# Kernel tuning notes

Measured on AMD Instinct MI355X. Metric: run time of the kernel, lower is better.

Reference implementation:

```python
import jax, jax.numpy as jnp
import numpy as np

B, T, IN_DIM, LATENT, NUM_TOKENS = 8, 2048, 1024, 256, 4096


def setup_inputs() -> dict:
    key = jax.random.key(0)
    k1, k2, k3 = jax.random.split(key, 3)
    x = jax.random.normal(k1, (B, T, IN_DIM), dtype=jnp.float32)
    # Linear projection params (Kaiming-ish scale)
    W = jax.random.normal(k2, (IN_DIM, LATENT), dtype=jnp.float32) / np.sqrt(IN_DIM)
    b = jnp.zeros((LATENT,), dtype=jnp.float32)
    # Codebook (nn.Embedding with xavier_uniform init ~ small normal here)
    codebook = jax.random.normal(k3, (NUM_TOKENS, LATENT), dtype=jnp.float32) * 0.05
    return {"x": x, "W": W, "b": b, "codebook": codebook}


def reference(x, W, b, codebook):
    # normalization='none' -> identity; projection: Linear(in_dim, latent_dim)
    h = jnp.einsum("btd,de->bte", x, W) + b              # [B,T,latent]
    flat = h.reshape(-1, h.shape[-1])                     # [N,latent]
    # cdist + argmin: squared distance gives identical argmin as euclidean
    # d2[n,k] = |flat[n]|^2 - 2 flat@cb^T + |cb[k]|^2
    d2 = (jnp.sum(flat * flat, axis=-1, keepdims=True)
          - 2.0 * (flat @ codebook.T)
          + jnp.sum(codebook * codebook, axis=-1))        # [N,num_tokens]
    indices = jnp.argmin(d2, axis=-1)                     # [N]
    codes = codebook[indices].reshape(h.shape)            # gather -> [B,T,latent]
    idx = indices.reshape(x.shape[:-1] + (1,))            # [B,T,1]
    return codes, idx
```

## Files before the change

kernel.cpp:

```cpp
#include <hip/hip_runtime.h>

#define NROWS   16384
#define INDIM   1024
#define KDIM    256
#define NCODES  4096
#define G_ROWS  32
#define V_ROWS  64
#define P_ROWS  128
#define NSTEP   128

#define VBUF    32768

#define MG_ROWS 64
#define MG_KC   64
#define MG_NCH  (INDIM / MG_KC)
#define XP(p)   ((p) * 8192)
#define WP(p)   (24576 + (p) * 32768)
#define MG_LDS  122880

typedef float f32x4 __attribute__((ext_vector_type(4)));
typedef int   i32x2 __attribute__((ext_vector_type(2)));
typedef short short8 __attribute__((ext_vector_type(8)));
typedef unsigned short u16x8 __attribute__((ext_vector_type(8)));
typedef unsigned short u16x4 __attribute__((ext_vector_type(4)));

__device__ inline unsigned short f2bf(float f) {
    unsigned u = __builtin_bit_cast(unsigned, f);
    u = (u + 0x7fffu + ((u >> 16) & 1u)) >> 16;
    return (unsigned short)u;
}
__device__ inline float bf2f(unsigned short h) {
    unsigned u = ((unsigned)h) << 16;
    return __builtin_bit_cast(float, u);
}
__device__ inline f32x4 mfma16(u16x8 a, u16x8 b, f32x4 c) {
    return __builtin_amdgcn_mfma_f32_16x16x32_bf16(
        __builtin_bit_cast(short8, a), __builtin_bit_cast(short8, b), c, 0, 0, 0);
}

__global__ __launch_bounds__(256) void wprep_kernel(const float* __restrict__ W,
                                                    unsigned short* __restrict__ wt_hi,
                                                    unsigned short* __restrict__ wt_md,
                                                    unsigned short* __restrict__ wt_lo) {
    const int t = threadIdx.x;
    const int k = blockIdx.x * 4 + (t >> 6);
    const int c0 = (t & 63) * 4;
    f32x4 v = *(const f32x4*)(W + (size_t)k * KDIM + c0);
    #pragma unroll
    for (int i = 0; i < 4; ++i) {
        const unsigned short h = f2bf(v[i]);
        const float r1 = v[i] - bf2f(h);
        const unsigned short m = f2bf(r1);
        const unsigned short lo = f2bf(r1 - bf2f(m));
        wt_hi[(size_t)(c0 + i) * INDIM + k] = h;
        wt_md[(size_t)(c0 + i) * INDIM + k] = m;
        wt_lo[(size_t)(c0 + i) * INDIM + k] = lo;
    }
}

__global__ __launch_bounds__(256, 1) void gemm_mfma_kernel(const float* __restrict__ x,
                                                           const unsigned short* __restrict__ wt_hi,
                                                           const unsigned short* __restrict__ wt_md,
                                                           const unsigned short* __restrict__ wt_lo,
                                                           const float* __restrict__ bvec,
                                                           float* __restrict__ hbuf) {
    __shared__ __align__(16) char lds[MG_LDS];

    const int t  = threadIdx.x;
    const int w  = t >> 6;
    const int l  = t & 63;
    const int nl = l & 15;
    const int g  = l >> 4;
    const size_t n0 = (size_t)blockIdx.x * MG_ROWS;
    const int lb = l * 16;

    f32x4 acc[4][4];
    #pragma unroll
    for (int a = 0; a < 4; ++a)
        #pragma unroll
        for (int b = 0; b < 4; ++b) acc[a][b] = (f32x4){0.f, 0.f, 0.f, 0.f};

    for (int kc = 0; kc < MG_NCH; ++kc) {
        f32x4 xa[2], xb[2];
        #pragma unroll
        for (int c = 0; c < 2; ++c) {
            const int idx = w * 2 + c;
            const int sX = idx >> 2, rsX = idx & 3;
            const float* p = x + (n0 + rsX * 16 + nl) * INDIM + kc * MG_KC + sX * 32 + g * 8;
            xa[c] = *(const f32x4*)(p);
            xb[c] = *(const f32x4*)(p + 4);
        }
        u16x8 wh[8], wm[8], wl[8];
        #pragma unroll
        for (int ci = 0; ci < 4; ++ci)
            #pragma unroll
            for (int sW = 0; sW < 2; ++sW) {
                const int q = ci * 2 + sW;
                const size_t off = (size_t)((w * 4 + ci) * 16 + nl) * INDIM
                                 + kc * MG_KC + sW * 32 + g * 8;
                wh[q] = *(const u16x8*)(wt_hi + off);
                wm[q] = *(const u16x8*)(wt_md + off);
                wl[q] = *(const u16x8*)(wt_lo + off);
            }
        __syncthreads();

        #pragma unroll
        for (int c = 0; c < 2; ++c) {
            const int idx = w * 2 + c;
            const int sX = idx >> 2, rsX = idx & 3;
            u16x8 xh, xm, xl;
            #pragma unroll
            for (int e = 0; e < 4; ++e) {
                const float a0 = xa[c][e], a1 = xb[c][e];
                const unsigned short h0 = f2bf(a0);
                const float r10 = a0 - bf2f(h0);
                const unsigned short m0 = f2bf(r10);
                const unsigned short l0 = f2bf(r10 - bf2f(m0));
                const unsigned short h1 = f2bf(a1);
                const float r11 = a1 - bf2f(h1);
                const unsigned short m1 = f2bf(r11);
                const unsigned short l1 = f2bf(r11 - bf2f(m1));
                xh[e] = h0; xh[4+e] = h1;
                xm[e] = m0; xm[4+e] = m1;
                xl[e] = l0; xl[4+e] = l1;
            }
            const int base = (sX * 4 + rsX) * 1024 + lb;
            *(u16x8*)(lds + XP(0) + base) = xh;
            *(u16x8*)(lds + XP(1) + base) = xm;
            *(u16x8*)(lds + XP(2) + base) = xl;
        }
        #pragma unroll
        for (int ci = 0; ci < 4; ++ci)
            #pragma unroll
            for (int sW = 0; sW < 2; ++sW) {
                const int q = ci * 2 + sW;
                const int base = (sW * 16 + w * 4 + ci) * 1024 + lb;
                *(u16x8*)(lds + WP(0) + base) = wh[q];
                *(u16x8*)(lds + WP(1) + base) = wm[q];
                *(u16x8*)(lds + WP(2) + base) = wl[q];
            }
        __syncthreads();

        #pragma unroll
        for (int s = 0; s < 2; ++s) {
            u16x8 bh[4], bm[4], bl[4], ah[4], am[4], al[4];
            #pragma unroll
            for (int rs = 0; rs < 4; ++rs) {
                const int base = (s * 4 + rs) * 1024 + lb;
                bh[rs] = *(const u16x8*)(lds + XP(0) + base);
                bm[rs] = *(const u16x8*)(lds + XP(1) + base);
                bl[rs] = *(const u16x8*)(lds + XP(2) + base);
            }
            #pragma unroll
            for (int ct = 0; ct < 4; ++ct) {
                const int base = (s * 16 + w * 4 + ct) * 1024 + lb;
                ah[ct] = *(const u16x8*)(lds + WP(0) + base);
                am[ct] = *(const u16x8*)(lds + WP(1) + base);
                al[ct] = *(const u16x8*)(lds + WP(2) + base);
            }
            #pragma unroll
            for (int ct = 0; ct < 4; ++ct)
                #pragma unroll
                for (int rs = 0; rs < 4; ++rs) {
                    acc[ct][rs] = mfma16(ah[ct], bh[rs], acc[ct][rs]);
                    acc[ct][rs] = mfma16(ah[ct], bm[rs], acc[ct][rs]);
                    acc[ct][rs] = mfma16(am[ct], bh[rs], acc[ct][rs]);
                    acc[ct][rs] = mfma16(ah[ct], bl[rs], acc[ct][rs]);
                    acc[ct][rs] = mfma16(al[ct], bh[rs], acc[ct][rs]);
                    acc[ct][rs] = mfma16(am[ct], bm[rs], acc[ct][rs]);
                }
        }
    }

    #pragma unroll
    for (int ct = 0; ct < 4; ++ct) {
        float bv[4];
        #pragma unroll
        for (int r = 0; r < 4; ++r) bv[r] = bvec[w * 64 + ct * 16 + g * 4 + r];
        #pragma unroll
        for (int rs = 0; rs < 4; ++rs) {
            const size_t row = n0 + rs * 16 + nl;
            #pragma unroll
            for (int r = 0; r < 4; ++r)
                hbuf[row * KDIM + w * 64 + ct * 16 + g * 4 + r] = acc[ct][rs][r] + bv[r];
        }
    }
}

__global__ __launch_bounds__(256, 2) void gemm_fb_kernel(const float* __restrict__ x,
                                                         const float* __restrict__ W,
                                                         const float* __restrict__ bvec,
                                                         float* __restrict__ hbuf) {
    const int t  = threadIdx.x;
    const int cg = t & 15;
    const int rg = t >> 4;
    const size_t n0 = (size_t)blockIdx.x * G_ROWS;
    const int c0 = cg * 16;

    float acc[2][16];
    #pragma unroll
    for (int j = 0; j < 2; ++j)
        #pragma unroll
        for (int cc = 0; cc < 16; ++cc) acc[j][cc] = 0.f;

    for (int k4 = 0; k4 < INDIM / 4; ++k4) {
        const int k = k4 * 4;
        f32x4 xv[2];
        #pragma unroll
        for (int j = 0; j < 2; ++j)
            xv[j] = *(const f32x4*)(x + (n0 + rg + 16 * j) * INDIM + k);
        f32x4 wv[4][4];
        #pragma unroll
        for (int kk = 0; kk < 4; ++kk)
            #pragma unroll
            for (int q = 0; q < 4; ++q)
                wv[kk][q] = *(const f32x4*)(W + (size_t)(k + kk) * KDIM + c0 + 4 * q);
        #pragma unroll
        for (int j = 0; j < 2; ++j)
            #pragma unroll
            for (int kk = 0; kk < 4; ++kk) {
                const float xs = xv[j][kk];
                #pragma unroll
                for (int q = 0; q < 4; ++q)
                    #pragma unroll
                    for (int e = 0; e < 4; ++e)
                        acc[j][4*q+e] = fmaf(xs, wv[kk][q][e], acc[j][4*q+e]);
            }
    }
    #pragma unroll
    for (int j = 0; j < 2; ++j) {
        float* dst = hbuf + (n0 + rg + 16 * j) * KDIM + c0;
        #pragma unroll
        for (int q = 0; q < 4; ++q) {
            f32x4 v;
            #pragma unroll
            for (int e = 0; e < 4; ++e) v[e] = acc[j][4*q+e] + bvec[c0 + 4*q + e];
            *(f32x4*)(dst + 4*q) = v;
        }
    }
}

__global__ __launch_bounds__(256) void prep_kernel(const float* __restrict__ cb,
                                                   float* __restrict__ cnorm,
                                                   unsigned short* __restrict__ cb_hi,
                                                   unsigned short* __restrict__ cb_lo,
                                                   int do_split) {
    const int c    = blockIdx.x * 4 + (threadIdx.x >> 6);
    const int lane = threadIdx.x & 63;
    f32x4 v = ((const f32x4*)(cb + (size_t)c * KDIM))[lane];
    if (do_split) {
        u16x4 h4, l4;
        #pragma unroll
        for (int j = 0; j < 4; ++j) {
            unsigned short h = f2bf(v[j]);
            h4[j] = h;
            l4[j] = f2bf(v[j] - bf2f(h));
        }
        *(u16x4*)(cb_hi + (size_t)c * KDIM + lane * 4) = h4;
        *(u16x4*)(cb_lo + (size_t)c * KDIM + lane * 4) = l4;
    }
    float s = v[0]*v[0] + v[1]*v[1] + v[2]*v[2] + v[3]*v[3];
    #pragma unroll
    for (int off = 1; off < 64; off <<= 1) s += __shfl_xor(s, off);
    if (lane == 0) cnorm[c] = s;
}

template<int PRE>
__global__ __launch_bounds__(256, 2) void vq_partial_kernel(
    const float* __restrict__ hbuf,
    const float* __restrict__ cb,
    const float* __restrict__ cnorm,
    const unsigned short* __restrict__ cb_hi,
    const unsigned short* __restrict__ cb_lo,
    int* __restrict__ recs)
{
    __shared__ __align__(16) char lds[2 * VBUF];

    const int t  = threadIdx.x;
    const int w  = t >> 6;
    const int l  = t & 63;
    const int nl = l & 15;
    const int g  = l >> 4;
    const int lb = l * 16;
    const int bid  = blockIdx.x;
    const int quar = bid & 3;
    const int S0   = quar * 32;
    const size_t n0 = (size_t)(bid >> 2) * P_ROWS;

    u16x8 bhi[2][8], bmid[2][8];
    #pragma unroll
    for (int rset = 0; rset < 2; ++rset) {
        const float* hrow = hbuf + (n0 + w * 32 + rset * 16 + nl) * KDIM;
        #pragma unroll
        for (int s = 0; s < 8; ++s) {
            f32x4 a = *(const f32x4*)(hrow + s * 32 + g * 8);
            f32x4 b = *(const f32x4*)(hrow + s * 32 + g * 8 + 4);
            u16x8 uh, um;
            #pragma unroll
            for (int jj = 0; jj < 4; ++jj) {
                unsigned short h0 = f2bf(a[jj]); uh[jj]   = h0; um[jj]   = f2bf(a[jj] - bf2f(h0));
                unsigned short h1 = f2bf(b[jj]); uh[4+jj] = h1; um[4+jj] = f2bf(b[jj] - bf2f(h1));
            }
            bhi[rset][s] = uh; bmid[rset][s] = um;
        }
    }

    float v1[2] = {3.4e38f, 3.4e38f}, v2[2] = {3.4e38f, 3.4e38f};
    int   i1[2] = {0, 0},            i2[2] = {0, 0};

    u16x8 rh[2][2], rl[2][2];

    #pragma unroll
    for (int t2 = 0; t2 < 2; ++t2)
        #pragma unroll
        for (int sv = 0; sv < 2; ++sv) {
            const int sst = w * 2 + sv;
            const int code = S0 * 32 + t2 * 16 + nl;
            if (PRE) {
                const size_t off = (size_t)code * KDIM + (sst * 4 + g) * 8;
                rh[t2][sv] = *(const u16x8*)(cb_hi + off);
                rl[t2][sv] = *(const u16x8*)(cb_lo + off);
            } else {
                const float* p = cb + (size_t)code * KDIM + (sst * 4 + g) * 8;
                f32x4 a = *(const f32x4*)(p);
                f32x4 b = *(const f32x4*)(p + 4);
                u16x8 uh, ul;
                #pragma unroll
                for (int jj = 0; jj < 4; ++jj) {
                    unsigned short h0 = f2bf(a[jj]); uh[jj]   = h0; ul[jj]   = f2bf(a[jj] - bf2f(h0));
                    unsigned short h1 = f2bf(b[jj]); uh[4+jj] = h1; ul[4+jj] = f2bf(b[jj] - bf2f(h1));
                }
                rh[t2][sv] = uh; rl[t2][sv] = ul;
            }
        }
    #pragma unroll
    for (int t2 = 0; t2 < 2; ++t2)
        #pragma unroll
        for (int sv = 0; sv < 2; ++sv) {
            const int base = (t2 * 8 + w * 2 + sv) * 1024 + lb;
            *(u16x8*)(lds + base) = rh[t2][sv];
            *(u16x8*)(lds + 16384 + base) = rl[t2][sv];
        }
    __syncthreads();

    for (int S = S0; S < S0 + 32; ++S) {
        const int b = S & 1;
        if (S + 1 < S0 + 32) {
            #pragma unroll
            for (int t2 = 0; t2 < 2; ++t2)
                #pragma unroll
                for (int sv = 0; sv < 2; ++sv) {
                    const int sst = w * 2 + sv;
                    const int code = (S + 1) * 32 + t2 * 16 + nl;
                    if (PRE) {
                        const size_t off = (size_t)code * KDIM + (sst * 4 + g) * 8;
                        rh[t2][sv] = *(const u16x8*)(cb_hi + off);
                        rl[t2][sv] = *(const u16x8*)(cb_lo + off);
                    } else {
                        const float* p = cb + (size_t)code * KDIM + (sst * 4 + g) * 8;
                        f32x4 a = *(const f32x4*)(p);
                        f32x4 bb = *(const f32x4*)(p + 4);
                        u16x8 uh, ul;
                        #pragma unroll
                        for (int jj = 0; jj < 4; ++jj) {
                            unsigned short h0 = f2bf(a[jj]);  uh[jj]   = h0; ul[jj]   = f2bf(a[jj] - bf2f(h0));
                            unsigned short h1 = f2bf(bb[jj]); uh[4+jj] = h1; ul[4+jj] = f2bf(bb[jj] - bf2f(h1));
                        }
                        rh[t2][sv] = uh; rl[t2][sv] = ul;
                    }
                }
        }
        f32x4 cn0 = *(const f32x4*)(cnorm + S * 32 + g * 4);
        f32x4 cn1 = *(const f32x4*)(cnorm + S * 32 + 16 + g * 4);
        {
            const char* buf = lds + b * VBUF;
            #pragma unroll
            for (int t2 = 0; t2 < 2; ++t2) {
                f32x4 acc0 = {0.f, 0.f, 0.f, 0.f};
                f32x4 acc1 = {0.f, 0.f, 0.f, 0.f};
                #pragma unroll
                for (int s = 0; s < 8; ++s) {
                    const int base = (t2 * 8 + s) * 1024 + lb;
                    u16x8 ahi = *(const u16x8*)(buf + base);
                    u16x8 alo = *(const u16x8*)(buf + 16384 + base);
                    acc0 = mfma16(ahi, bhi[0][s],  acc0);
                    acc0 = mfma16(ahi, bmid[0][s], acc0);
                    acc0 = mfma16(alo, bhi[0][s],  acc0);
                    acc1 = mfma16(ahi, bhi[1][s],  acc1);
                    acc1 = mfma16(ahi, bmid[1][s], acc1);
                    acc1 = mfma16(alo, bhi[1][s],  acc1);
                }
                const f32x4 cn = t2 ? cn1 : cn0;
                #pragma unroll
                for (int r = 0; r < 4; ++r) {
                    const int c = S * 32 + t2 * 16 + g * 4 + r;
                    const float d0 = cn[r] - 2.0f * acc0[r];
                    if (d0 < v1[0])      { v2[0] = v1[0]; i2[0] = i1[0]; v1[0] = d0; i1[0] = c; }
                    else if (d0 < v2[0]) { v2[0] = d0; i2[0] = c; }
                    const float d1 = cn[r] - 2.0f * acc1[r];
                    if (d1 < v1[1])      { v2[1] = v1[1]; i2[1] = i1[1]; v1[1] = d1; i1[1] = c; }
                    else if (d1 < v2[1]) { v2[1] = d1; i2[1] = c; }
                }
            }
        }
        __syncthreads();
        if (S + 1 < S0 + 32) {
            char* nbuf = lds + (b ^ 1) * VBUF;
            #pragma unroll
            for (int t2 = 0; t2 < 2; ++t2)
                #pragma unroll
                for (int sv = 0; sv < 2; ++sv) {
                    const int base = (t2 * 8 + w * 2 + sv) * 1024 + lb;
                    *(u16x8*)(nbuf + base) = rh[t2][sv];
                    *(u16x8*)(nbuf + 16384 + base) = rl[t2][sv];
                }
        }
        __syncthreads();
    }

    #pragma unroll
    for (int rset = 0; rset < 2; ++rset) {
        #pragma unroll
        for (int off = 16; off <= 32; off <<= 1) {
            float ov1 = __shfl_xor(v1[rset], off); int oi1 = __shfl_xor(i1[rset], off);
            float ov2 = __shfl_xor(v2[rset], off); int oi2 = __shfl_xor(i2[rset], off);
            if (ov1 < v1[rset] || (ov1 == v1[rset] && oi1 < i1[rset])) {
                float tv = v1[rset]; int ti = i1[rset]; v1[rset] = ov1; i1[rset] = oi1; ov1 = tv; oi1 = ti;
                tv = v2[rset]; ti = i2[rset]; v2[rset] = ov2; i2[rset] = oi2; ov2 = tv; oi2 = ti;
            }
            if (ov1 < v2[rset] || (ov1 == v2[rset] && oi1 < i2[rset])) { v2[rset] = ov1; i2[rset] = oi1; }
        }
    }

    if (g == 0) {
        #pragma unroll
        for (int rset = 0; rset < 2; ++rset) {
            i32x2 rec;
            rec[0] = i1[rset]; rec[1] = i2[rset];
            const size_t row = n0 + w * 32 + rset * 16 + nl;
            *(i32x2*)(recs + (row * 4 + quar) * 2) = rec;
        }
    }
}

__global__ __launch_bounds__(256) void vq_merge_kernel(
    float* __restrict__ hbuf,
    const float* __restrict__ cb,
    const float* __restrict__ cnorm,
    const int* __restrict__ recs,
    float* __restrict__ idx_out)
{
    const int t  = threadIdx.x;
    const int w  = t >> 6;
    const int l  = t & 63;
    const int nl = l & 15;
    const int g  = l >> 4;
    const size_t n0 = (size_t)blockIdx.x * V_ROWS;
    const int row = w * 16 + nl;
    float* hrow = hbuf + (n0 + row) * KDIM;

    int cand[8];
    {
        const size_t rb = (n0 + row) * 8;
        #pragma unroll
        for (int q = 0; q < 4; ++q) {
            i32x2 rq = *(const i32x2*)(recs + rb + q * 2);
            int a = rq[0], b = rq[1];
            cand[2*q]   = (a < 0) ? 0 : (a > NCODES - 1 ? NCODES - 1 : a);
            cand[2*q+1] = (b < 0) ? 0 : (b > NCODES - 1 ? NCODES - 1 : b);
        }
    }

    f32x4 hreg[16];
    #pragma unroll
    for (int s = 0; s < 8; ++s) {
        hreg[2*s]   = *(const f32x4*)(hrow + s * 32 + g * 8);
        hreg[2*s+1] = *(const f32x4*)(hrow + s * 32 + g * 8 + 4);
    }

    float bestd = 3.4e38f;
    int   besti = 0x7fffffff;
    #pragma unroll
    for (int k = 0; k < 8; ++k) {
        const int ci = cand[k];
        const float* cp = cb + (size_t)ci * KDIM;
        float d = 0.f;
        #pragma unroll
        for (int s = 0; s < 8; ++s) {
            f32x4 a = *(const f32x4*)(cp + s * 32 + g * 8);
            f32x4 b = *(const f32x4*)(cp + s * 32 + g * 8 + 4);
            #pragma unroll
            for (int jj = 0; jj < 4; ++jj) {
                d = fmaf(a[jj], hreg[2*s][jj], d);
                d = fmaf(b[jj], hreg[2*s+1][jj], d);
            }
        }
        d += __shfl_xor(d, 16); d += __shfl_xor(d, 32);
        const float d2 = cnorm[ci] - 2.f * d;
        if (d2 < bestd || (d2 == bestd && ci < besti)) { bestd = d2; besti = ci; }
    }

    const float* cw = cb + (size_t)besti * KDIM;
    #pragma unroll
    for (int s = 0; s < 8; ++s) {
        *(f32x4*)(hrow + s * 32 + g * 8)     = *(const f32x4*)(cw + s * 32 + g * 8);
        *(f32x4*)(hrow + s * 32 + g * 8 + 4) = *(const f32x4*)(cw + s * 32 + g * 8 + 4);
    }
    if (g == 0) idx_out[n0 + row] = (float)besti;
}

template<int PRE>
__global__ __launch_bounds__(256) void vq_kernel(
    float* __restrict__ hbuf,
    const float* __restrict__ cb,
    const float* __restrict__ cnorm,
    const unsigned short* __restrict__ cb_hi,
    const unsigned short* __restrict__ cb_lo,
    float* __restrict__ idx_out)
{
    __shared__ __align__(16) char lds[2 * VBUF];

    const int t  = threadIdx.x;
    const int w  = t >> 6;
    const int l  = t & 63;
    const int nl = l & 15;
    const int g  = l >> 4;
    const int lb = l * 16;
    const size_t n0 = (size_t)blockIdx.x * V_ROWS;
    const int row = w * 16 + nl;
    float* hrow = hbuf + (n0 + row) * KDIM;

    u16x8 bhi[8], bmid[8];
    #pragma unroll
    for (int s = 0; s < 8; ++s) {
        f32x4 a = *(const f32x4*)(hrow + s * 32 + g * 8);
        f32x4 b = *(const f32x4*)(hrow + s * 32 + g * 8 + 4);
        u16x8 uh, um;
        #pragma unroll
        for (int jj = 0; jj < 4; ++jj) {
            unsigned short h0 = f2bf(a[jj]); uh[jj]   = h0; um[jj]   = f2bf(a[jj] - bf2f(h0));
            unsigned short h1 = f2bf(b[jj]); uh[4+jj] = h1; um[4+jj] = f2bf(b[jj] - bf2f(h1));
        }
        bhi[s] = uh; bmid[s] = um;
    }

    float v1 = 3.4e38f, v2 = 3.4e38f;
    int   i1 = 0, i2 = 0;

    u16x8 rh[2][2], rl[2][2];

    #pragma unroll
    for (int t2 = 0; t2 < 2; ++t2)
        #pragma unroll
        for (int sv = 0; sv < 2; ++sv) {
            const int sst = w * 2 + sv;
            if (PRE) {
                const size_t off = (size_t)(t2 * 16 + nl) * KDIM + (sst * 4 + g) * 8;
                rh[t2][sv] = *(const u16x8*)(cb_hi + off);
                rl[t2][sv] = *(const u16x8*)(cb_lo + off);
            } else {
                const float* p = cb + (size_t)(t2 * 16 + nl) * KDIM + (sst * 4 + g) * 8;
                f32x4 a = *(const f32x4*)(p);
                f32x4 b = *(const f32x4*)(p + 4);
                u16x8 uh, ul;
                #pragma unroll
                for (int jj = 0; jj < 4; ++jj) {
                    unsigned short h0 = f2bf(a[jj]); uh[jj]   = h0; ul[jj]   = f2bf(a[jj] - bf2f(h0));
                    unsigned short h1 = f2bf(b[jj]); uh[4+jj] = h1; ul[4+jj] = f2bf(b[jj] - bf2f(h1));
                }
                rh[t2][sv] = uh; rl[t2][sv] = ul;
            }
        }
    #pragma unroll
    for (int t2 = 0; t2 < 2; ++t2)
        #pragma unroll
        for (int sv = 0; sv < 2; ++sv) {
            const int base = (t2 * 8 + w * 2 + sv) * 1024 + lb;
            *(u16x8*)(lds + base) = rh[t2][sv];
            *(u16x8*)(lds + 16384 + base) = rl[t2][sv];
        }
    __syncthreads();

    for (int S = 0; S < NSTEP; ++S) {
        const int b = S & 1;
        if (S + 1 < NSTEP) {
            #pragma unroll
            for (int t2 = 0; t2 < 2; ++t2)
                #pragma unroll
                for (int sv = 0; sv < 2; ++sv) {
                    const int sst = w * 2 + sv;
                    const int code = (S + 1) * 32 + t2 * 16 + nl;
                    if (PRE) {
                        const size_t off = (size_t)code * KDIM + (sst * 4 + g) * 8;
                        rh[t2][sv] = *(const u16x8*)(cb_hi + off);
                        rl[t2][sv] = *(const u16x8*)(cb_lo + off);
                    } else {
                        const float* p = cb + (size_t)code * KDIM + (sst * 4 + g) * 8;
                        f32x4 a = *(const f32x4*)(p);
                        f32x4 bb = *(const f32x4*)(p + 4);
                        u16x8 uh, ul;
                        #pragma unroll
                        for (int jj = 0; jj < 4; ++jj) {
                            unsigned short h0 = f2bf(a[jj]);  uh[jj]   = h0; ul[jj]   = f2bf(a[jj] - bf2f(h0));
                            unsigned short h1 = f2bf(bb[jj]); uh[4+jj] = h1; ul[4+jj] = f2bf(bb[jj] - bf2f(h1));
                        }
                        rh[t2][sv] = uh; rl[t2][sv] = ul;
                    }
                }
        }
        f32x4 cn0 = *(const f32x4*)(cnorm + S * 32 + g * 4);
        f32x4 cn1 = *(const f32x4*)(cnorm + S * 32 + 16 + g * 4);
        {
            const char* buf = lds + b * VBUF;
            #pragma unroll
            for (int t2 = 0; t2 < 2; ++t2) {
                f32x4 acc = {0.f, 0.f, 0.f, 0.f};
                #pragma unroll
                for (int s = 0; s < 8; ++s) {
                    const int base = (t2 * 8 + s) * 1024 + lb;
                    u16x8 ahi = *(const u16x8*)(buf + base);
                    u16x8 alo = *(const u16x8*)(buf + 16384 + base);
                    acc = mfma16(ahi, bhi[s],  acc);
                    acc = mfma16(ahi, bmid[s], acc);
                    acc = mfma16(alo, bhi[s],  acc);
                }
                const f32x4 cn = t2 ? cn1 : cn0;
                #pragma unroll
                for (int r = 0; r < 4; ++r) {
                    const float d2 = cn[r] - 2.0f * acc[r];
                    const int c = S * 32 + t2 * 16 + g * 4 + r;
                    if (d2 < v1)      { v2 = v1; i2 = i1; v1 = d2; i1 = c; }
                    else if (d2 < v2) { v2 = d2; i2 = c; }
                }
            }
        }
        __syncthreads();
        if (S + 1 < NSTEP) {
            char* nbuf = lds + (b ^ 1) * VBUF;
            #pragma unroll
            for (int t2 = 0; t2 < 2; ++t2)
                #pragma unroll
                for (int sv = 0; sv < 2; ++sv) {
                    const int base = (t2 * 8 + w * 2 + sv) * 1024 + lb;
                    *(u16x8*)(nbuf + base) = rh[t2][sv];
                    *(u16x8*)(nbuf + 16384 + base) = rl[t2][sv];
                }
        }
        __syncthreads();
    }

    #pragma unroll
    for (int off = 16; off <= 32; off <<= 1) {
        float ov1 = __shfl_xor(v1, off); int oi1 = __shfl_xor(i1, off);
        float ov2 = __shfl_xor(v2, off); int oi2 = __shfl_xor(i2, off);
        if (ov1 < v1 || (ov1 == v1 && oi1 < i1)) {
            float tv = v1; int ti = i1; v1 = ov1; i1 = oi1; ov1 = tv; oi1 = ti;
            tv = v2; ti = i2; v2 = ov2; i2 = oi2; ov2 = tv; oi2 = ti;
        }
        if (ov1 < v2 || (ov1 == v2 && oi1 < i2)) { v2 = ov1; i2 = oi1; }
    }

    i1 = (i1 < 0) ? 0 : (i1 > NCODES - 1 ? NCODES - 1 : i1);
    i2 = (i2 < 0) ? 0 : (i2 > NCODES - 1 ? NCODES - 1 : i2);

    const float* cp1 = cb + (size_t)i1 * KDIM;
    const float* cp2 = cb + (size_t)i2 * KDIM;
    float da = 0.f, db = 0.f;
    #pragma unroll
    for (int s = 0; s < 8; ++s) {
        f32x4 h0 = *(const f32x4*)(hrow + s * 32 + g * 8);
        f32x4 h1 = *(const f32x4*)(hrow + s * 32 + g * 8 + 4);
        f32x4 a1 = *(const f32x4*)(cp1 + s * 32 + g * 8);
        f32x4 b1 = *(const f32x4*)(cp1 + s * 32 + g * 8 + 4);
        f32x4 a2 = *(const f32x4*)(cp2 + s * 32 + g * 8);
        f32x4 b2 = *(const f32x4*)(cp2 + s * 32 + g * 8 + 4);
        #pragma unroll
        for (int jj = 0; jj < 4; ++jj) {
            da = fmaf(a1[jj], h0[jj], da); da = fmaf(b1[jj], h1[jj], da);
            db = fmaf(a2[jj], h0[jj], db); db = fmaf(b2[jj], h1[jj], db);
        }
    }
    da += __shfl_xor(da, 16); da += __shfl_xor(da, 32);
    db += __shfl_xor(db, 16); db += __shfl_xor(db, 32);
    const float d2a = cnorm[i1] - 2.f * da;
    const float d2b = cnorm[i2] - 2.f * db;
    const int win = (d2a < d2b || (d2a == d2b && i1 < i2)) ? i1 : i2;

    const float* cw = cb + (size_t)win * KDIM;
    #pragma unroll
    for (int s = 0; s < 8; ++s) {
        *(f32x4*)(hrow + s * 32 + g * 8)     = *(const f32x4*)(cw + s * 32 + g * 8);
        *(f32x4*)(hrow + s * 32 + g * 8 + 4) = *(const f32x4*)(cw + s * 32 + g * 8 + 4);
    }
    if (g == 0) idx_out[n0 + row] = (float)win;
}

extern "C" void kernel_launch(void* const* d_in, const int* in_sizes, int n_in,
                              void* d_out, int out_size, void* d_ws, size_t ws_size,
                              hipStream_t stream) {
    (void)in_sizes; (void)n_in; (void)out_size;
    const float* x    = (const float*)d_in[0];
    const float* W    = (const float*)d_in[1];
    const float* bvec = (const float*)d_in[2];
    const float* cb   = (const float*)d_in[3];

    float* codes_out = (float*)d_out;
    float* idx_out   = (float*)d_out + (size_t)NROWS * KDIM;

    float* cnorm = (float*)d_ws;
    int*   recs  = (int*)((char*)d_ws + 16384);
    unsigned short* cb_hi = (unsigned short*)((char*)d_ws + 16384 + 524288);
    unsigned short* cb_lo = cb_hi + (size_t)NCODES * KDIM;
    unsigned short* wt_hi = cb_lo + (size_t)NCODES * KDIM;
    unsigned short* wt_md = wt_hi + (size_t)INDIM * KDIM;
    unsigned short* wt_lo = wt_md + (size_t)INDIM * KDIM;

    const size_t need_rec  = 16384 + 524288;
    const size_t need_cb   = need_rec + (size_t)NCODES * KDIM * 2 * sizeof(unsigned short);
    const size_t need_full = need_cb + (size_t)INDIM * KDIM * 3 * sizeof(unsigned short);

    const int use_split = (ws_size >= need_rec) ? 1 : 0;
    const int pre_cb    = (ws_size >= need_cb) ? 1 : 0;
    const int fast_g    = (ws_size >= need_full) ? 1 : 0;

    if (fast_g) {
        wprep_kernel<<<INDIM / 4, 256, 0, stream>>>(W, wt_hi, wt_md, wt_lo);
        gemm_mfma_kernel<<<NROWS / MG_ROWS, 256, 0, stream>>>(x, wt_hi, wt_md, wt_lo, bvec, codes_out);
    } else {
        gemm_fb_kernel<<<NROWS / G_ROWS, 256, 0, stream>>>(x, W, bvec, codes_out);
    }
    prep_kernel<<<NCODES / 4, 256, 0, stream>>>(cb, cnorm, cb_hi, cb_lo, pre_cb);

    if (use_split) {
        if (pre_cb)
            vq_partial_kernel<1><<<(NROWS / P_ROWS) * 4, 256, 0, stream>>>(codes_out, cb, cnorm, cb_hi, cb_lo, recs);
        else
            vq_partial_kernel<0><<<(NROWS / P_ROWS) * 4, 256, 0, stream>>>(codes_out, cb, cnorm, cb_hi, cb_lo, recs);
        vq_merge_kernel<<<NROWS / V_ROWS, 256, 0, stream>>>(codes_out, cb, cnorm, recs, idx_out);
    } else {
        if (pre_cb)
            vq_kernel<1><<<NROWS / V_ROWS, 256, 0, stream>>>(codes_out, cb, cnorm, cb_hi, cb_lo, idx_out);
        else
            vq_kernel<0><<<NROWS / V_ROWS, 256, 0, stream>>>(codes_out, cb, cnorm, cb_hi, cb_lo, idx_out);
    }
}
```

Baseline: 262.3 us.

## Use direct global-to-LDS loads with smaller codebook tiles in VQ partial kernel

The partial VQ search kernel now streams 16 codes per step instead of 32, which halves its LDS footprint. The launch bound rises from 2 to 4 blocks per CU. In the precomputed path, codebook hi/lo tiles are fetched with global_load_lds, so data goes straight to shared memory without passing through registers, and the second barrier per step is dropped. The aim is to raise occupancy and cut register and LDS-store traffic, at the cost of twice as many loop iterations and barriers per block.

```diff
diff --git a/kernel.cpp b/kernel.cpp
--- a/kernel.cpp
+++ b/kernel.cpp
@@ -7,8 +7,10 @@
 #define G_ROWS  32
 #define V_ROWS  64
 #define P_ROWS  128
+#define PSTEP   64
 #define NSTEP   128
 
+#define PVBUF   16384
 #define VBUF    32768
 
 #define MG_ROWS 64
@@ -36,6 +38,13 @@
 __device__ inline f32x4 mfma16(u16x8 a, u16x8 b, f32x4 c) {
     return __builtin_amdgcn_mfma_f32_16x16x32_bf16(
         __builtin_bit_cast(short8, a), __builtin_bit_cast(short8, b), c, 0, 0, 0);
+}
+
+__device__ inline void gload16(const void* g, void* l) {
+    __builtin_amdgcn_global_load_lds(
+        (const __attribute__((address_space(1))) unsigned int*)g,
+        (__attribute__((address_space(3))) unsigned int*)l,
+        16, 0, 0);
 }
 
 __global__ __launch_bounds__(256) void wprep_kernel(const float* __restrict__ W,
@@ -266,7 +275,7 @@
 }
 
 template<int PRE>
-__global__ __launch_bounds__(256, 2) void vq_partial_kernel(
+__global__ __launch_bounds__(256, 4) void vq_partial_kernel(
     const float* __restrict__ hbuf,
     const float* __restrict__ cb,
     const float* __restrict__ cnorm,
@@ -274,7 +283,7 @@
     const unsigned short* __restrict__ cb_lo,
     int* __restrict__ recs)
 {
-    __shared__ __align__(16) char lds[2 * VBUF];
+    __shared__ __align__(16) char lds[2 * PVBUF];
 
     const int t  = threadIdx.x;
     const int w  = t >> 6;
@@ -284,7 +293,7 @@
     const int lb = l * 16;
     const int bid  = blockIdx.x;
     const int quar = bid & 3;
-    const int S0   = quar * 32;
+    const int cbase = quar * 1024;
     const size_t n0 = (size_t)(bid >> 2) * P_ROWS;
 
     u16x8 bhi[2][8], bmid[2][8];
@@ -308,6 +317,240 @@
     float v1[2] = {3.4e38f, 3.4e38f}, v2[2] = {3.4e38f, 3.4e38f};
     int   i1[2] = {0, 0},            i2[2] = {0, 0};
 
+    u16x8 rh[2], rl[2];
+
+    if (PRE) {
+        #pragma unroll
+        for (int sv = 0; sv < 2; ++sv) {
+            const int sc = w * 2 + sv;
+            const size_t off = (size_t)(cbase + nl) * KDIM + (sc * 4 + g) * 8;
+            gload16(cb_hi + off, lds + sc * 1024);
+            gload16(cb_lo + off, lds + 8192 + sc * 1024);
+        }
+    } else {
+        #pragma unroll
+        for (int sv = 0; sv < 2; ++sv) {
+            const int sc = w * 2 + sv;
+            const float* p = cb + (size_t)(cbase + nl) * KDIM + (sc * 4 + g) * 8;
+            f32x4 a = *(const f32x4*)(p);
+            f32x4 b = *(const f32x4*)(p + 4);
+            u16x8 uh, ul;
+            #pragma unroll
+            for (int jj = 0; jj < 4; ++jj) {
+                unsigned short h0 = f2bf(a[jj]); uh[jj]   = h0; ul[jj]   = f2bf(a[jj] - bf2f(h0));
+                unsigned short h1 = f2bf(b[jj]); uh[4+jj] = h1; ul[4+jj] = f2bf(b[jj] - bf2f(h1));
+            }
+            rh[sv] = uh; rl[sv] = ul;
+        }
+        #pragma unroll
+        for (int sv = 0; sv < 2; ++sv) {
+            const int sc = w * 2 + sv;
+            *(u16x8*)(lds + sc * 1024 + lb) = rh[sv];
+            *(u16x8*)(lds + 8192 + sc * 1024 + lb) = rl[sv];
+        }
+    }
+    __syncthreads();
+
+    for (int S = 0; S < PSTEP; ++S) {
+        const int b = S & 1;
+        char* nbuf = lds + (b ^ 1) * PVBUF;
+        if (S + 1 < PSTEP) {
+            if (PRE) {
+                #pragma unroll
+                for (int sv = 0; sv < 2; ++sv) {
+                    const int sc = w * 2 + sv;
+                    const size_t off = (size_t)(cbase + (S + 1) * 16 + nl) * KDIM + (sc * 4 + g) * 8;
+                    gload16(cb_hi + off, nbuf + sc * 1024);
+                    gload16(cb_lo + off, nbuf + 8192 + sc * 1024);
+                }
+            } else {
+                #pragma unroll
+                for (int sv = 0; sv < 2; ++sv) {
+                    const int sc = w * 2 + sv;
+                    const float* p = cb + (size_t)(cbase + (S + 1) * 16 + nl) * KDIM + (sc * 4 + g) * 8;
+                    f32x4 a = *(const f32x4*)(p);
+                    f32x4 bb = *(const f32x4*)(p + 4);
+                    u16x8 uh, ul;
+                    #pragma unroll
+                    for (int jj = 0; jj < 4; ++jj) {
+                        unsigned short h0 = f2bf(a[jj]);  uh[jj]   = h0; ul[jj]   = f2bf(a[jj] - bf2f(h0));
+                        unsigned short h1 = f2bf(bb[jj]); uh[4+jj] = h1; ul[4+jj] = f2bf(bb[jj] - bf2f(h1));
+                    }
+                    rh[sv] = uh; rl[sv] = ul;
+                }
+            }
+        }
+        const f32x4 cn = *(const f32x4*)(cnorm + cbase + S * 16 + g * 4);
+        {
+            const char* buf = lds + b * PVBUF;
+            f32x4 acc0 = {0.f, 0.f, 0.f, 0.f};
+            f32x4 acc1 = {0.f, 0.f, 0.f, 0.f};
+            #pragma unroll
+            for (int s = 0; s < 8; ++s) {
+                const int base = s * 1024 + lb;
+                u16x8 ahi = *(const u16x8*)(buf + base);
+                u16x8 alo = *(const u16x8*)(buf + 8192 + base);
+                acc0 = mfma16(ahi, bhi[0][s],  acc0);
+                acc0 = mfma16(ahi, bmid[0][s], acc0);
+                acc0 = mfma16(alo, bhi[0][s],  acc0);
+                acc1 = mfma16(ahi, bhi[1][s],  acc1);
+                acc1 = mfma16(ahi, bmid[1][s], acc1);
+                acc1 = mfma16(alo, bhi[1][s],  acc1);
+            }
+            #pragma unroll
+            for (int r = 0; r < 4; ++r) {
+                const int c = cbase + S * 16 + g * 4 + r;
+                const float d0 = cn[r] - 2.0f * acc0[r];
+                if (d0 < v1[0])      { v2[0] = v1[0]; i2[0] = i1[0]; v1[0] = d0; i1[0] = c; }
+                else if (d0 < v2[0]) { v2[0] = d0; i2[0] = c; }
+                const float d1 = cn[r] - 2.0f * acc1[r];
+                if (d1 < v1[1])      { v2[1] = v1[1]; i2[1] = i1[1]; v1[1] = d1; i1[1] = c; }
+                else if (d1 < v2[1]) { v2[1] = d1; i2[1] = c; }
+            }
+        }
+        __syncthreads();
+        if (!PRE) {
+            if (S + 1 < PSTEP) {
+                #pragma unroll
+                for (int sv = 0; sv < 2; ++sv) {
+                    const int sc = w * 2 + sv;
+                    *(u16x8*)(nbuf + sc * 1024 + lb) = rh[sv];
+                    *(u16x8*)(nbuf + 8192 + sc * 1024 + lb) = rl[sv];
+                }
+            }
+            __syncthreads();
+        }
+    }
+
+    #pragma unroll
+    for (int rset = 0; rset < 2; ++rset) {
+        #pragma unroll
+        for (int off = 16; off <= 32; off <<= 1) {
+            float ov1 = __shfl_xor(v1[rset], off); int oi1 = __shfl_xor(i1[rset], off);
+            float ov2 = __shfl_xor(v2[rset], off); int oi2 = __shfl_xor(i2[rset], off);
+            if (ov1 < v1[rset] || (ov1 == v1[rset] && oi1 < i1[rset])) {
+                float tv = v1[rset]; int ti = i1[rset]; v1[rset] = ov1; i1[rset] = oi1; ov1 = tv; oi1 = ti;
+                tv = v2[rset]; ti = i2[rset]; v2[rset] = ov2; i2[rset] = oi2; ov2 = tv; oi2 = ti;
+            }
+            if (ov1 < v2[rset] || (ov1 == v2[rset] && oi1 < i2[rset])) { v2[rset] = ov1; i2[rset] = oi1; }
+        }
+    }
+
+    if (g == 0) {
+        #pragma unroll
+        for (int rset = 0; rset < 2; ++rset) {
+            i32x2 rec;
+            rec[0] = i1[rset]; rec[1] = i2[rset];
+            const size_t row = n0 + w * 32 + rset * 16 + nl;
+            *(i32x2*)(recs + (row * 4 + quar) * 2) = rec;
+        }
+    }
+}
+
+__global__ __launch_bounds__(256) void vq_merge_kernel(
+    float* __restrict__ hbuf,
+    const float* __restrict__ cb,
+    const float* __restrict__ cnorm,
+    const int* __restrict__ recs,
+    float* __restrict__ idx_out)
+{
+    const int t  = threadIdx.x;
+    const int w  = t >> 6;
+    const int l  = t & 63;
+    const int nl = l & 15;
+    const int g  = l >> 4;
+    const size_t n0 = (size_t)blockIdx.x * V_ROWS;
+    const int row = w * 16 + nl;
+    float* hrow = hbuf + (n0 + row) * KDIM;
+
+    int cand[8];
+    {
+        const size_t rb = (n0 + row) * 8;
+        #pragma unroll
+        for (int q = 0; q < 4; ++q) {
+            i32x2 rq = *(const i32x2*)(recs + rb + q * 2);
+            int a = rq[0], b = rq[1];
+            cand[2*q]   = (a < 0) ? 0 : (a > NCODES - 1 ? NCODES - 1 : a);
+            cand[2*q+1] = (b < 0) ? 0 : (b > NCODES - 1 ? NCODES - 1 : b);
+        }
+    }
+
+    f32x4 hreg[16];
+    #pragma unroll
+    for (int s = 0; s < 8; ++s) {
+        hreg[2*s]   = *(const f32x4*)(hrow + s * 32 + g * 8);
+        hreg[2*s+1] = *(const f32x4*)(hrow + s * 32 + g * 8 + 4);
+    }
+
+    float bestd = 3.4e38f;
+    int   besti = 0x7fffffff;
+    #pragma unroll
+    for (int k = 0; k < 8; ++k) {
+        const int ci = cand[k];
+        const float* cp = cb + (size_t)ci * KDIM;
+        float d = 0.f;
+        #pragma unroll
+        for (int s = 0; s < 8; ++s) {
+            f32x4 a = *(const f32x4*)(cp + s * 32 + g * 8);
+            f32x4 b = *(const f32x4*)(cp + s * 32 + g * 8 + 4);
+            #pragma unroll
+            for (int jj = 0; jj < 4; ++jj) {
+                d = fmaf(a[jj], hreg[2*s][jj], d);
+                d = fmaf(b[jj], hreg[2*s+1][jj], d);
+            }
+        }
+        d += __shfl_xor(d, 16); d += __shfl_xor(d, 32);
+        const float d2 = cnorm[ci] - 2.f * d;
+        if (d2 < bestd || (d2 == bestd && ci < besti)) { bestd = d2; besti = ci; }
+    }
+
+    const float* cw = cb + (size_t)besti * KDIM;
+    #pragma unroll
+    for (int s = 0; s < 8; ++s) {
+        *(f32x4*)(hrow + s * 32 + g * 8)     = *(const f32x4*)(cw + s * 32 + g * 8);
+        *(f32x4*)(hrow + s * 32 + g * 8 + 4) = *(const f32x4*)(cw + s * 32 + g * 8 + 4);
+    }
+    if (g == 0) idx_out[n0 + row] = (float)besti;
+}
+
+template<int PRE>
+__global__ __launch_bounds__(256) void vq_kernel(
+    float* __restrict__ hbuf,
+    const float* __restrict__ cb,
+    const float* __restrict__ cnorm,
+    const unsigned short* __restrict__ cb_hi,
+    const unsigned short* __restrict__ cb_lo,
+    float* __restrict__ idx_out)
+{
+    __shared__ __align__(16) char lds[2 * VBUF];
+
+    const int t  = threadIdx.x;
+    const int w  = t >> 6;
+    const int l  = t & 63;
+    const int nl = l & 15;
+    const int g  = l >> 4;
+    const int lb = l * 16;
+    const size_t n0 = (size_t)blockIdx.x * V_ROWS;
+    const int row = w * 16 + nl;
+    float* hrow = hbuf + (n0 + row) * KDIM;
+
+    u16x8 bhi[8], bmid[8];
+    #pragma unroll
+    for (int s = 0; s < 8; ++s) {
+        f32x4 a = *(const f32x4*)(hrow + s * 32 + g * 8);
+        f32x4 b = *(const f32x4*)(hrow + s * 32 + g * 8 + 4);
+        u16x8 uh, um;
+        #pragma unroll
+        for (int jj = 0; jj < 4; ++jj) {
+            unsigned short h0 = f2bf(a[jj]); uh[jj]   = h0; um[jj]   = f2bf(a[jj] - bf2f(h0));
+            unsigned short h1 = f2bf(b[jj]); uh[4+jj] = h1; um[4+jj] = f2bf(b[jj] - bf2f(h1));
+        }
+        bhi[s] = uh; bmid[s] = um;
+    }
+
+    float v1 = 3.4e38f, v2 = 3.4e38f;
+    int   i1 = 0, i2 = 0;
+
     u16x8 rh[2][2], rl[2][2];
 
     #pragma unroll
@@ -315,13 +558,12 @@
         #pragma unroll
         for (int sv = 0; sv < 2; ++sv) {
             const int sst = w * 2 + sv;
-            const int code = S0 * 32 + t2 * 16 + nl;
             if (PRE) {
-                const size_t off = (size_t)code * KDIM + (sst * 4 + g) * 8;
+                const size_t off = (size_t)(t2 * 16 + nl) * KDIM + (sst * 4 + g) * 8;
                 rh[t2][sv] = *(const u16x8*)(cb_hi + off);
                 rl[t2][sv] = *(const u16x8*)(cb_lo + off);
             } else {
-                const float* p = cb + (size_t)code * KDIM + (sst * 4 + g) * 8;
+                const float* p = cb + (size_t)(t2 * 16 + nl) * KDIM + (sst * 4 + g) * 8;
                 f32x4 a = *(const f32x4*)(p);
                 f32x4 b = *(const f32x4*)(p + 4);
                 u16x8 uh, ul;
@@ -343,9 +585,9 @@
         }
     __syncthreads();
 
-    for (int S = S0; S < S0 + 32; ++S) {
+    for (int S = 0; S < NSTEP; ++S) {
         const int b = S & 1;
-        if (S + 1 < S0 + 32) {
+        if (S + 1 < NSTEP) {
             #pragma unroll
             for (int t2 = 0; t2 < 2; ++t2)
                 #pragma unroll
@@ -376,244 +618,6 @@
             const char* buf = lds + b * VBUF;
             #pragma unroll
             for (int t2 = 0; t2 < 2; ++t2) {
-                f32x4 acc0 = {0.f, 0.f, 0.f, 0.f};
-                f32x4 acc1 = {0.f, 0.f, 0.f, 0.f};
-                #pragma unroll
-                for (int s = 0; s < 8; ++s) {
-                    const int base = (t2 * 8 + s) * 1024 + lb;
-                    u16x8 ahi = *(const u16x8*)(buf + base);
-                    u16x8 alo = *(const u16x8*)(buf + 16384 + base);
-                    acc0 = mfma16(ahi, bhi[0][s],  acc0);
-                    acc0 = mfma16(ahi, bmid[0][s], acc0);
-                    acc0 = mfma16(alo, bhi[0][s],  acc0);
-                    acc1 = mfma16(ahi, bhi[1][s],  acc1);
-                    acc1 = mfma16(ahi, bmid[1][s], acc1);
-                    acc1 = mfma16(alo, bhi[1][s],  acc1);
-                }
-                const f32x4 cn = t2 ? cn1 : cn0;
-                #pragma unroll
-                for (int r = 0; r < 4; ++r) {
-                    const int c = S * 32 + t2 * 16 + g * 4 + r;
-                    const float d0 = cn[r] - 2.0f * acc0[r];
-                    if (d0 < v1[0])      { v2[0] = v1[0]; i2[0] = i1[0]; v1[0] = d0; i1[0] = c; }
-                    else if (d0 < v2[0]) { v2[0] = d0; i2[0] = c; }
-                    const float d1 = cn[r] - 2.0f * acc1[r];
-                    if (d1 < v1[1])      { v2[1] = v1[1]; i2[1] = i1[1]; v1[1] = d1; i1[1] = c; }
-                    else if (d1 < v2[1]) { v2[1] = d1; i2[1] = c; }
-                }
-            }
-        }
-        __syncthreads();
-        if (S + 1 < S0 + 32) {
-            char* nbuf = lds + (b ^ 1) * VBUF;
-            #pragma unroll
-            for (int t2 = 0; t2 < 2; ++t2)
-                #pragma unroll
-                for (int sv = 0; sv < 2; ++sv) {
-                    const int base = (t2 * 8 + w * 2 + sv) * 1024 + lb;
-                    *(u16x8*)(nbuf + base) = rh[t2][sv];
-                    *(u16x8*)(nbuf + 16384 + base) = rl[t2][sv];
-                }
-        }
-        __syncthreads();
-    }
-
-    #pragma unroll
-    for (int rset = 0; rset < 2; ++rset) {
-        #pragma unroll
-        for (int off = 16; off <= 32; off <<= 1) {
-            float ov1 = __shfl_xor(v1[rset], off); int oi1 = __shfl_xor(i1[rset], off);
-            float ov2 = __shfl_xor(v2[rset], off); int oi2 = __shfl_xor(i2[rset], off);
-            if (ov1 < v1[rset] || (ov1 == v1[rset] && oi1 < i1[rset])) {
-                float tv = v1[rset]; int ti = i1[rset]; v1[rset] = ov1; i1[rset] = oi1; ov1 = tv; oi1 = ti;
-                tv = v2[rset]; ti = i2[rset]; v2[rset] = ov2; i2[rset] = oi2; ov2 = tv; oi2 = ti;
-            }
-            if (ov1 < v2[rset] || (ov1 == v2[rset] && oi1 < i2[rset])) { v2[rset] = ov1; i2[rset] = oi1; }
-        }
-    }
-
-    if (g == 0) {
-        #pragma unroll
-        for (int rset = 0; rset < 2; ++rset) {
-            i32x2 rec;
-            rec[0] = i1[rset]; rec[1] = i2[rset];
-            const size_t row = n0 + w * 32 + rset * 16 + nl;
-            *(i32x2*)(recs + (row * 4 + quar) * 2) = rec;
-        }
-    }
-}
-
-__global__ __launch_bounds__(256) void vq_merge_kernel(
-    float* __restrict__ hbuf,
-    const float* __restrict__ cb,
-    const float* __restrict__ cnorm,
-    const int* __restrict__ recs,
-    float* __restrict__ idx_out)
-{
-    const int t  = threadIdx.x;
-    const int w  = t >> 6;
-    const int l  = t & 63;
-    const int nl = l & 15;
-    const int g  = l >> 4;
-    const size_t n0 = (size_t)blockIdx.x * V_ROWS;
-    const int row = w * 16 + nl;
-    float* hrow = hbuf + (n0 + row) * KDIM;
-
-    int cand[8];
-    {
-        const size_t rb = (n0 + row) * 8;
-        #pragma unroll
-        for (int q = 0; q < 4; ++q) {
-            i32x2 rq = *(const i32x2*)(recs + rb + q * 2);
-            int a = rq[0], b = rq[1];
-            cand[2*q]   = (a < 0) ? 0 : (a > NCODES - 1 ? NCODES - 1 : a);
-            cand[2*q+1] = (b < 0) ? 0 : (b > NCODES - 1 ? NCODES - 1 : b);
-        }
-    }
-
-    f32x4 hreg[16];
-    #pragma unroll
-    for (int s = 0; s < 8; ++s) {
-        hreg[2*s]   = *(const f32x4*)(hrow + s * 32 + g * 8);
-        hreg[2*s+1] = *(const f32x4*)(hrow + s * 32 + g * 8 + 4);
-    }
-
-    float bestd = 3.4e38f;
-    int   besti = 0x7fffffff;
-    #pragma unroll
-    for (int k = 0; k < 8; ++k) {
-        const int ci = cand[k];
-        const float* cp = cb + (size_t)ci * KDIM;
-        float d = 0.f;
-        #pragma unroll
-        for (int s = 0; s < 8; ++s) {
-            f32x4 a = *(const f32x4*)(cp + s * 32 + g * 8);
-            f32x4 b = *(const f32x4*)(cp + s * 32 + g * 8 + 4);
-            #pragma unroll
-            for (int jj = 0; jj < 4; ++jj) {
-                d = fmaf(a[jj], hreg[2*s][jj], d);
-                d = fmaf(b[jj], hreg[2*s+1][jj], d);
-            }
-        }
-        d += __shfl_xor(d, 16); d += __shfl_xor(d, 32);
-        const float d2 = cnorm[ci] - 2.f * d;
-        if (d2 < bestd || (d2 == bestd && ci < besti)) { bestd = d2; besti = ci; }
-    }
-
-    const float* cw = cb + (size_t)besti * KDIM;
-    #pragma unroll
-    for (int s = 0; s < 8; ++s) {
-        *(f32x4*)(hrow + s * 32 + g * 8)     = *(const f32x4*)(cw + s * 32 + g * 8);
-        *(f32x4*)(hrow + s * 32 + g * 8 + 4) = *(const f32x4*)(cw + s * 32 + g * 8 + 4);
-    }
-    if (g == 0) idx_out[n0 + row] = (float)besti;
-}
-
-template<int PRE>
-__global__ __launch_bounds__(256) void vq_kernel(
-    float* __restrict__ hbuf,
-    const float* __restrict__ cb,
-    const float* __restrict__ cnorm,
-    const unsigned short* __restrict__ cb_hi,
-    const unsigned short* __restrict__ cb_lo,
-    float* __restrict__ idx_out)
-{
-    __shared__ __align__(16) char lds[2 * VBUF];
-
-    const int t  = threadIdx.x;
-    const int w  = t >> 6;
-    const int l  = t & 63;
-    const int nl = l & 15;
-    const int g  = l >> 4;
-    const int lb = l * 16;
-    const size_t n0 = (size_t)blockIdx.x * V_ROWS;
-    const int row = w * 16 + nl;
-    float* hrow = hbuf + (n0 + row) * KDIM;
-
-    u16x8 bhi[8], bmid[8];
-    #pragma unroll
-    for (int s = 0; s < 8; ++s) {
-        f32x4 a = *(const f32x4*)(hrow + s * 32 + g * 8);
-        f32x4 b = *(const f32x4*)(hrow + s * 32 + g * 8 + 4);
-        u16x8 uh, um;
-        #pragma unroll
-        for (int jj = 0; jj < 4; ++jj) {
-            unsigned short h0 = f2bf(a[jj]); uh[jj]   = h0; um[jj]   = f2bf(a[jj] - bf2f(h0));
-            unsigned short h1 = f2bf(b[jj]); uh[4+jj] = h1; um[4+jj] = f2bf(b[jj] - bf2f(h1));
-        }
-        bhi[s] = uh; bmid[s] = um;
-    }
-
-    float v1 = 3.4e38f, v2 = 3.4e38f;
-    int   i1 = 0, i2 = 0;
-
-    u16x8 rh[2][2], rl[2][2];
-
-    #pragma unroll
-    for (int t2 = 0; t2 < 2; ++t2)
-        #pragma unroll
-        for (int sv = 0; sv < 2; ++sv) {
-            const int sst = w * 2 + sv;
-            if (PRE) {
-                const size_t off = (size_t)(t2 * 16 + nl) * KDIM + (sst * 4 + g) * 8;
-                rh[t2][sv] = *(const u16x8*)(cb_hi + off);
-                rl[t2][sv] = *(const u16x8*)(cb_lo + off);
-            } else {
-                const float* p = cb + (size_t)(t2 * 16 + nl) * KDIM + (sst * 4 + g) * 8;
-                f32x4 a = *(const f32x4*)(p);
-                f32x4 b = *(const f32x4*)(p + 4);
-                u16x8 uh, ul;
-                #pragma unroll
-                for (int jj = 0; jj < 4; ++jj) {
-                    unsigned short h0 = f2bf(a[jj]); uh[jj]   = h0; ul[jj]   = f2bf(a[jj] - bf2f(h0));
-                    unsigned short h1 = f2bf(b[jj]); uh[4+jj] = h1; ul[4+jj] = f2bf(b[jj] - bf2f(h1));
-                }
-                rh[t2][sv] = uh; rl[t2][sv] = ul;
-            }
-        }
-    #pragma unroll
-    for (int t2 = 0; t2 < 2; ++t2)
-        #pragma unroll
-        for (int sv = 0; sv < 2; ++sv) {
-            const int base = (t2 * 8 + w * 2 + sv) * 1024 + lb;
-            *(u16x8*)(lds + base) = rh[t2][sv];
-            *(u16x8*)(lds + 16384 + base) = rl[t2][sv];
-        }
-    __syncthreads();
-
-    for (int S = 0; S < NSTEP; ++S) {
-        const int b = S & 1;
-        if (S + 1 < NSTEP) {
-            #pragma unroll
-            for (int t2 = 0; t2 < 2; ++t2)
-                #pragma unroll
-                for (int sv = 0; sv < 2; ++sv) {
-                    const int sst = w * 2 + sv;
-                    const int code = (S + 1) * 32 + t2 * 16 + nl;
-                    if (PRE) {
-                        const size_t off = (size_t)code * KDIM + (sst * 4 + g) * 8;
-                        rh[t2][sv] = *(const u16x8*)(cb_hi + off);
-                        rl[t2][sv] = *(const u16x8*)(cb_lo + off);
-                    } else {
-                        const float* p = cb + (size_t)code * KDIM + (sst * 4 + g) * 8;
-                        f32x4 a = *(const f32x4*)(p);
-                        f32x4 bb = *(const f32x4*)(p + 4);
-                        u16x8 uh, ul;
-                        #pragma unroll
-                        for (int jj = 0; jj < 4; ++jj) {
-                            unsigned short h0 = f2bf(a[jj]);  uh[jj]   = h0; ul[jj]   = f2bf(a[jj] - bf2f(h0));
-                            unsigned short h1 = f2bf(bb[jj]); uh[4+jj] = h1; ul[4+jj] = f2bf(bb[jj] - bf2f(h1));
-                        }
-                        rh[t2][sv] = uh; rl[t2][sv] = ul;
-                    }
-                }
-        }
-        f32x4 cn0 = *(const f32x4*)(cnorm + S * 32 + g * 4);
-        f32x4 cn1 = *(const f32x4*)(cnorm + S * 32 + 16 + g * 4);
-        {
-            const char* buf = lds + b * VBUF;
-            #pragma unroll
-            for (int t2 = 0; t2 < 2; ++t2) {
                 f32x4 acc = {0.f, 0.f, 0.f, 0.f};
                 #pragma unroll
                 for (int s = 0; s < 8; ++s) {
```

Result: slower. 487.9 us (+86.0%).
